# Kernel tuning notes

Hardware: AMD Instinct MI355X
Metric: run time of the kernel (lower is better)

Reference implementation:

```python
import jax, jax.numpy as jnp
import numpy as np

M, N, B, S = 512, 1024, 64, 50   # measurements, signal dim, batch, sparsity
TAU, ETA = 1.0, 0.1


def setup_inputs() -> dict:
    key = jax.random.key(0)
    k1, k2, k3 = jax.random.split(key, 3)
    X = jax.random.normal(k1, (N, B), dtype=jnp.float32)
    Y = jax.random.normal(k2, (B, M), dtype=jnp.float32)
    A = jax.random.normal(k3, (M, N), dtype=jnp.float32) / np.sqrt(M).astype(np.float32)
    W = jnp.ones((N,), dtype=jnp.float32)
    return {"X": X, "Y": Y, "A": A, "W": W}


def reference(X, Y, A, W):
    # Gradient step: H1 = (I - eta A^T A) X + eta A^T Y^T, computed without
    # materializing the N x N operator.  H1: (N, B)
    H1 = X - ETA * (A.T @ (A @ X)) + ETA * (A.T @ Y.T)
    # NeuralSort soft top-s mask per sample, batched over B.
    z = jnp.abs(W[:, None] * H1).T                      # (B, N) scores
    c = jnp.sum(jnp.abs(z[:, :, None] - z[:, None, :]), axis=-1)  # (B, N)
    ks = (N + 1 - 2 * jnp.arange(1, S + 1)).astype(z.dtype)       # (S,)
    logits = (ks[None, :, None] * z[:, None, :] - c[:, None, :]) / TAU  # (B, S, N)
    mask = jnp.sum(jax.nn.softmax(logits, axis=-1), axis=1)            # (B, N)
    return mask.T * H1                                  # (N, B)
```

## Files before the change

kernel.cpp:

```cpp
#include <hip/hip_runtime.h>
#include <math.h>

#define MM 512
#define NN 1024
#define BB 64
#define SS 50
#define ETA 0.1f

__global__ __launch_bounds__(512) void k_r(const float* __restrict__ X,
                                           const float* __restrict__ Y,
                                           const float* __restrict__ A,
                                           float* __restrict__ R_t) {
  const int l = threadIdx.x;
  const int w = threadIdx.y;
  const int m0 = blockIdx.x * 2;
  __shared__ float part[8][2][BB];
  const float* __restrict__ Xp = X + w * 128 * BB + l;
  const float* __restrict__ A0 = A + (size_t)m0 * NN + w * 128;
  const float* __restrict__ A1 = A0 + NN;
  float r0a = 0.f, r0b = 0.f, r1a = 0.f, r1b = 0.f;
  #pragma unroll 8
  for (int i = 0; i < 128; i += 4) {
    const float x0 = Xp[(i + 0) * BB];
    const float x1 = Xp[(i + 1) * BB];
    const float x2 = Xp[(i + 2) * BB];
    const float x3 = Xp[(i + 3) * BB];
    const float4 a0 = *reinterpret_cast<const float4*>(A0 + i);
    const float4 a1 = *reinterpret_cast<const float4*>(A1 + i);
    r0a = fmaf(a0.x, x0, fmaf(a0.y, x1, r0a));
    r0b = fmaf(a0.z, x2, fmaf(a0.w, x3, r0b));
    r1a = fmaf(a1.x, x0, fmaf(a1.y, x1, r1a));
    r1b = fmaf(a1.z, x2, fmaf(a1.w, x3, r1b));
  }
  part[w][0][l] = r0a + r0b;
  part[w][1][l] = r1a + r1b;
  __syncthreads();
  if (w == 0) {
    const float s0 =
        ((part[0][0][l] + part[1][0][l]) + (part[2][0][l] + part[3][0][l])) +
        ((part[4][0][l] + part[5][0][l]) + (part[6][0][l] + part[7][0][l]));
    const float s1 =
        ((part[0][1][l] + part[1][1][l]) + (part[2][1][l] + part[3][1][l])) +
        ((part[4][1][l] + part[5][1][l]) + (part[6][1][l] + part[7][1][l]));
    const float2 y2 = *reinterpret_cast<const float2*>(Y + l * MM + m0);
    *reinterpret_cast<float2*>(R_t + l * MM + m0) =
        make_float2(y2.x - s0, y2.y - s1);
  }
}

__global__ __launch_bounds__(512) void k_h1z(const float* __restrict__ X,
                                             const float* __restrict__ A,
                                             const float* __restrict__ R_t,
                                             const float* __restrict__ W,
                                             float* __restrict__ H1_t,
                                             float* __restrict__ z_t) {
  const int l = threadIdx.x;
  const int w = threadIdx.y;
  const int nc = blockIdx.x & 7;
  const int bp = blockIdx.x >> 3;
  const int t5 = w * 64 + l;
  __shared__ __align__(16) float Rs[2][MM];
  __shared__ float p2[2][4][128];

  if (t5 < 256) {
    const int row = t5 >> 7;
    const int idx = t5 & 127;
    reinterpret_cast<float4*>(Rs[row])[idx] =
        reinterpret_cast<const float4*>(R_t + (size_t)(bp * 2 + row) * MM)[idx];
  }
  __syncthreads();

  const int b_l = w >> 2;
  const int mc = w & 3;
  const int n0 = nc * 128;
  const float2* __restrict__ A2 =
      reinterpret_cast<const float2*>(A) + (size_t)(mc * 128) * (NN / 2) + n0 / 2 + l;
  const float4* __restrict__ R4 =
      reinterpret_cast<const float4*>(Rs[b_l]) + mc * 32;
  float s0 = 0.f, s1 = 0.f, s2 = 0.f, s3 = 0.f;
  float u0 = 0.f, u1 = 0.f, u2 = 0.f, u3 = 0.f;
  #pragma unroll 2
  for (int i = 0; i < 128; i += 4) {
    const float4 r = R4[i >> 2];
    const float2 q0 = A2[(size_t)(i + 0) * (NN / 2)];
    const float2 q1 = A2[(size_t)(i + 1) * (NN / 2)];
    const float2 q2 = A2[(size_t)(i + 2) * (NN / 2)];
    const float2 q3 = A2[(size_t)(i + 3) * (NN / 2)];
    s0 = fmaf(q0.x, r.x, s0); u0 = fmaf(q0.y, r.x, u0);
    s1 = fmaf(q1.x, r.y, s1); u1 = fmaf(q1.y, r.y, u1);
    s2 = fmaf(q2.x, r.z, s2); u2 = fmaf(q2.y, r.z, u2);
    s3 = fmaf(q3.x, r.w, s3); u3 = fmaf(q3.y, r.w, u3);
  }
  p2[b_l][mc][l * 2 + 0] = (s0 + s1) + (s2 + s3);
  p2[b_l][mc][l * 2 + 1] = (u0 + u1) + (u2 + u3);
  __syncthreads();
  if (t5 < 256) {
    const int bl2 = t5 >> 7;
    const int nn = t5 & 127;
    const int bb = bp * 2 + bl2;
    const int n = n0 + nn;
    const float s = (p2[bl2][0][nn] + p2[bl2][1][nn]) +
                    (p2[bl2][2][nn] + p2[bl2][3][nn]);
    const float h = fmaf(ETA, s, X[n * BB + bb]);
    H1_t[bb * NN + n] = h;
    z_t[bb * NN + n] = fabsf(W[n] * h);
  }
}

__global__ __launch_bounds__(256) void k_c(const float* __restrict__ z_t,
                                           float* __restrict__ c_part) {
  const int b = blockIdx.x >> 2;
  const int q = blockIdx.x & 3;
  const int t = threadIdx.x;
  __shared__ __align__(16) float4 z4[NN / 4];
  z4[t] = reinterpret_cast<const float4*>(z_t + b * NN)[t];
  __syncthreads();
  const float* zs = reinterpret_cast<const float*>(z4);
  const float zn0 = zs[t];
  const float zn1 = zs[t + 256];
  const float zn2 = zs[t + 512];
  const float zn3 = zs[t + 768];
  float c0 = 0.f, c1 = 0.f, c2 = 0.f, c3 = 0.f;
  const float4* zq = z4 + q * 64;
  #pragma unroll 4
  for (int i = 0; i < 64; ++i) {
    const float4 f = zq[i];
    c0 += (fabsf(zn0 - f.x) + fabsf(zn0 - f.y)) + (fabsf(zn0 - f.z) + fabsf(zn0 - f.w));
    c1 += (fabsf(zn1 - f.x) + fabsf(zn1 - f.y)) + (fabsf(zn1 - f.z) + fabsf(zn1 - f.w));
    c2 += (fabsf(zn2 - f.x) + fabsf(zn2 - f.y)) + (fabsf(zn2 - f.z) + fabsf(zn2 - f.w));
    c3 += (fabsf(zn3 - f.x) + fabsf(zn3 - f.y)) + (fabsf(zn3 - f.z) + fabsf(zn3 - f.w));
  }
  float* cp = c_part + (size_t)(b * 4 + q) * NN;
  cp[t] = c0;
  cp[t + 256] = c1;
  cp[t + 512] = c2;
  cp[t + 768] = c3;
}

__global__ __launch_bounds__(1024) void k_sm(const float* __restrict__ z_t,
                                             const float* __restrict__ c_part,
                                             const float* __restrict__ H1_t,
                                             float* __restrict__ out) {
  const int b = blockIdx.x;
  const int t = threadIdx.x;
  __shared__ __align__(16) float2 zc_s[NN];
  __shared__ float mpart[16][NN];

  const float* __restrict__ cb = c_part + (size_t)b * 4 * NN;
  const float c = (cb[t] + cb[t + NN]) + (cb[t + 2 * NN] + cb[t + 3 * NN]);
  zc_s[t] = make_float2(z_t[b * NN + t], c);
  const float h = H1_t[b * NN + t];
  __syncthreads();

  const int w = t >> 6;
  const int lane = t & 63;
  float zz[16], cc[16], mp[16];
  #pragma unroll
  for (int k = 0; k < 16; ++k) {
    const float2 v = zc_s[lane + 64 * k];
    zz[k] = v.x;
    cc[k] = v.y;
    mp[k] = 0.f;
  }

  for (int s = w; s < SS; s += 16) {
    const float ks = (float)(NN + 1 - 2 * (s + 1));
    float lg[16];
    float mx = -INFINITY;
    #pragma unroll
    for (int k = 0; k < 16; ++k) {
      lg[k] = fmaf(ks, zz[k], -cc[k]);
      mx = fmaxf(mx, lg[k]);
    }
    #pragma unroll
    for (int off = 32; off > 0; off >>= 1)
      mx = fmaxf(mx, __shfl_xor(mx, off, 64));
    float sum = 0.f;
    #pragma unroll
    for (int k = 0; k < 16; ++k) {
      lg[k] = __expf(lg[k] - mx);
      sum += lg[k];
    }
    #pragma unroll
    for (int off = 32; off > 0; off >>= 1)
      sum += __shfl_xor(sum, off, 64);
    const float rs = 1.f / sum;
    #pragma unroll
    for (int k = 0; k < 16; ++k) mp[k] = fmaf(lg[k], rs, mp[k]);
  }
  #pragma unroll
  for (int k = 0; k < 16; ++k) mpart[w][lane + 64 * k] = mp[k];
  __syncthreads();

  float mask = 0.f;
  #pragma unroll
  for (int u = 0; u < 16; ++u) mask += mpart[u][t];
  out[t * BB + b] = mask * h;
}

extern "C" void kernel_launch(void* const* d_in, const int* in_sizes, int n_in,
                              void* d_out, int out_size, void* d_ws, size_t ws_size,
                              hipStream_t stream) {
  const float* X = (const float*)d_in[0];
  const float* Y = (const float*)d_in[1];
  const float* A = (const float*)d_in[2];
  const float* W = (const float*)d_in[3];
  float* out = (float*)d_out;

  float* R_t = (float*)d_ws;
  float* z_t = R_t + BB * MM;
  float* H1_t = z_t + BB * NN;
  float* c_part = H1_t + BB * NN;

  k_r   <<<dim3(MM / 2), dim3(64, 8), 0, stream>>>(X, Y, A, R_t);
  k_h1z <<<dim3(256), dim3(64, 8), 0, stream>>>(X, A, R_t, W, H1_t, z_t);
  k_c   <<<dim3(BB * 4), dim3(256), 0, stream>>>(z_t, c_part);
  k_sm  <<<dim3(BB), dim3(1024), 0, stream>>>(z_t, c_part, H1_t, out);
}
```

Measured before the change: 35.69 us.

## Fuse H1, pairwise-distance and softmax stages into one dataflow kernel with counters

Merges the three kernels after the residual stage into a single launch. Block ranges play the producer or consumer role for each stage and hand off through device-scope atomic counters with spin-waits, which removes two launch gaps and lets later stages begin per batch column as soon as their inputs are ready. The k_r kernel zeroes the counters. The change depends on producer blocks being scheduled before or alongside the consumers that spin on them, and on all 576 blocks fitting co-resident on the device. Stores use atomic exchange and loads use atomic loads, which may cost more than plain memory ops. The softmax stage now uses 512 threads per block instead of 1024.

```diff
diff --git a/kernel.cpp b/kernel.cpp
--- a/kernel.cpp
+++ b/kernel.cpp
@@ -6,14 +6,38 @@
 #define BB 64
 #define SS 50
 #define ETA 0.1f
+#define AGENT __HIP_MEMORY_SCOPE_AGENT
+
+#define P_C0 256
+#define P_S0 512
+#define NPIPE 576
+
+__device__ __forceinline__ float aload(const float* p) {
+  return __hip_atomic_load(p, __ATOMIC_RELAXED, AGENT);
+}
+__device__ __forceinline__ void xstore(float* p, float v) {
+  (void)__hip_atomic_exchange(p, v, __ATOMIC_RELAXED, AGENT);
+}
+__device__ __forceinline__ void bump(unsigned* p) {
+  __hip_atomic_fetch_add(p, 1u, __ATOMIC_RELAXED, AGENT);
+}
+__device__ __forceinline__ void spin_ge(const unsigned* p, unsigned tgt) {
+  while (__hip_atomic_load(p, __ATOMIC_RELAXED, AGENT) < tgt)
+    __builtin_amdgcn_s_sleep(2);
+}
 
 __global__ __launch_bounds__(512) void k_r(const float* __restrict__ X,
                                            const float* __restrict__ Y,
                                            const float* __restrict__ A,
-                                           float* __restrict__ R_t) {
+                                           float* __restrict__ R_t,
+                                           unsigned* __restrict__ cnt) {
   const int l = threadIdx.x;
   const int w = threadIdx.y;
   const int m0 = blockIdx.x * 2;
+  if (blockIdx.x == 0) {
+    const int tid = w * 64 + l;
+    if (tid < 96) __hip_atomic_store(&cnt[tid], 0u, __ATOMIC_RELAXED, AGENT);
+  }
   __shared__ float part[8][2][BB];
   const float* __restrict__ Xp = X + w * 128 * BB + l;
   const float* __restrict__ A0 = A + (size_t)m0 * NN + w * 128;
@@ -48,154 +72,167 @@
   }
 }
 
-__global__ __launch_bounds__(512) void k_h1z(const float* __restrict__ X,
-                                             const float* __restrict__ A,
-                                             const float* __restrict__ R_t,
-                                             const float* __restrict__ W,
-                                             float* __restrict__ H1_t,
-                                             float* __restrict__ z_t) {
-  const int l = threadIdx.x;
-  const int w = threadIdx.y;
-  const int nc = blockIdx.x & 7;
-  const int bp = blockIdx.x >> 3;
-  const int t5 = w * 64 + l;
-  __shared__ __align__(16) float Rs[2][MM];
-  __shared__ float p2[2][4][128];
-
-  if (t5 < 256) {
-    const int row = t5 >> 7;
-    const int idx = t5 & 127;
-    reinterpret_cast<float4*>(Rs[row])[idx] =
-        reinterpret_cast<const float4*>(R_t + (size_t)(bp * 2 + row) * MM)[idx];
-  }
-  __syncthreads();
-
-  const int b_l = w >> 2;
-  const int mc = w & 3;
-  const int n0 = nc * 128;
-  const float2* __restrict__ A2 =
-      reinterpret_cast<const float2*>(A) + (size_t)(mc * 128) * (NN / 2) + n0 / 2 + l;
-  const float4* __restrict__ R4 =
-      reinterpret_cast<const float4*>(Rs[b_l]) + mc * 32;
-  float s0 = 0.f, s1 = 0.f, s2 = 0.f, s3 = 0.f;
-  float u0 = 0.f, u1 = 0.f, u2 = 0.f, u3 = 0.f;
-  #pragma unroll 2
-  for (int i = 0; i < 128; i += 4) {
-    const float4 r = R4[i >> 2];
-    const float2 q0 = A2[(size_t)(i + 0) * (NN / 2)];
-    const float2 q1 = A2[(size_t)(i + 1) * (NN / 2)];
-    const float2 q2 = A2[(size_t)(i + 2) * (NN / 2)];
-    const float2 q3 = A2[(size_t)(i + 3) * (NN / 2)];
-    s0 = fmaf(q0.x, r.x, s0); u0 = fmaf(q0.y, r.x, u0);
-    s1 = fmaf(q1.x, r.y, s1); u1 = fmaf(q1.y, r.y, u1);
-    s2 = fmaf(q2.x, r.z, s2); u2 = fmaf(q2.y, r.z, u2);
-    s3 = fmaf(q3.x, r.w, s3); u3 = fmaf(q3.y, r.w, u3);
-  }
-  p2[b_l][mc][l * 2 + 0] = (s0 + s1) + (s2 + s3);
-  p2[b_l][mc][l * 2 + 1] = (u0 + u1) + (u2 + u3);
-  __syncthreads();
-  if (t5 < 256) {
-    const int bl2 = t5 >> 7;
-    const int nn = t5 & 127;
-    const int bb = bp * 2 + bl2;
-    const int n = n0 + nn;
-    const float s = (p2[bl2][0][nn] + p2[bl2][1][nn]) +
-                    (p2[bl2][2][nn] + p2[bl2][3][nn]);
-    const float h = fmaf(ETA, s, X[n * BB + bb]);
-    H1_t[bb * NN + n] = h;
-    z_t[bb * NN + n] = fabsf(W[n] * h);
-  }
-}
-
-__global__ __launch_bounds__(256) void k_c(const float* __restrict__ z_t,
-                                           float* __restrict__ c_part) {
-  const int b = blockIdx.x >> 2;
-  const int q = blockIdx.x & 3;
+__global__ __launch_bounds__(512, 6) void k_pipe(
+    const float* __restrict__ X,
+    const float* __restrict__ A,
+    const float* __restrict__ R_t,
+    const float* __restrict__ W,
+    float* __restrict__ z_t,
+    float* __restrict__ H1_t,
+    float* __restrict__ c_part,
+    unsigned* __restrict__ cnt,
+    float* __restrict__ out) {
+  __shared__ __align__(16) char smem[40960];
+  const int bid = blockIdx.x;
   const int t = threadIdx.x;
-  __shared__ __align__(16) float4 z4[NN / 4];
-  z4[t] = reinterpret_cast<const float4*>(z_t + b * NN)[t];
-  __syncthreads();
-  const float* zs = reinterpret_cast<const float*>(z4);
-  const float zn0 = zs[t];
-  const float zn1 = zs[t + 256];
-  const float zn2 = zs[t + 512];
-  const float zn3 = zs[t + 768];
-  float c0 = 0.f, c1 = 0.f, c2 = 0.f, c3 = 0.f;
-  const float4* zq = z4 + q * 64;
-  #pragma unroll 4
-  for (int i = 0; i < 64; ++i) {
-    const float4 f = zq[i];
-    c0 += (fabsf(zn0 - f.x) + fabsf(zn0 - f.y)) + (fabsf(zn0 - f.z) + fabsf(zn0 - f.w));
-    c1 += (fabsf(zn1 - f.x) + fabsf(zn1 - f.y)) + (fabsf(zn1 - f.z) + fabsf(zn1 - f.w));
-    c2 += (fabsf(zn2 - f.x) + fabsf(zn2 - f.y)) + (fabsf(zn2 - f.z) + fabsf(zn2 - f.w));
-    c3 += (fabsf(zn3 - f.x) + fabsf(zn3 - f.y)) + (fabsf(zn3 - f.z) + fabsf(zn3 - f.w));
-  }
-  float* cp = c_part + (size_t)(b * 4 + q) * NN;
-  cp[t] = c0;
-  cp[t + 256] = c1;
-  cp[t + 512] = c2;
-  cp[t + 768] = c3;
-}
-
-__global__ __launch_bounds__(1024) void k_sm(const float* __restrict__ z_t,
-                                             const float* __restrict__ c_part,
-                                             const float* __restrict__ H1_t,
-                                             float* __restrict__ out) {
-  const int b = blockIdx.x;
-  const int t = threadIdx.x;
-  __shared__ __align__(16) float2 zc_s[NN];
-  __shared__ float mpart[16][NN];
-
-  const float* __restrict__ cb = c_part + (size_t)b * 4 * NN;
-  const float c = (cb[t] + cb[t + NN]) + (cb[t + 2 * NN] + cb[t + 3 * NN]);
-  zc_s[t] = make_float2(z_t[b * NN + t], c);
-  const float h = H1_t[b * NN + t];
-  __syncthreads();
-
+  const int l = t & 63;
   const int w = t >> 6;
-  const int lane = t & 63;
-  float zz[16], cc[16], mp[16];
-  #pragma unroll
-  for (int k = 0; k < 16; ++k) {
-    const float2 v = zc_s[lane + 64 * k];
-    zz[k] = v.x;
-    cc[k] = v.y;
-    mp[k] = 0.f;
-  }
-
-  for (int s = w; s < SS; s += 16) {
-    const float ks = (float)(NN + 1 - 2 * (s + 1));
-    float lg[16];
-    float mx = -INFINITY;
+  unsigned* cnt_h = cnt;
+  unsigned* cnt_c = cnt + 32;
+
+  if (bid < P_C0) {
+    const int nc = bid & 7;
+    const int bp = bid >> 3;
+    float* Rs = reinterpret_cast<float*>(smem);
+    float(*p2)[4][128] = reinterpret_cast<float(*)[4][128]>(smem + 4096);
+    Rs[t] = R_t[(size_t)(bp * 2) * MM + t];
+    Rs[512 + t] = R_t[(size_t)(bp * 2 + 1) * MM + t];
+    __syncthreads();
+    const int b_l = w >> 2;
+    const int mc = w & 3;
+    const int n0 = nc * 128;
+    const float2* __restrict__ A2 =
+        reinterpret_cast<const float2*>(A) + (size_t)(mc * 128) * (NN / 2) + n0 / 2 + l;
+    const float4* __restrict__ R4 =
+        reinterpret_cast<const float4*>(Rs + b_l * MM) + mc * 32;
+    float s0 = 0.f, s1 = 0.f, s2 = 0.f, s3 = 0.f;
+    float u0 = 0.f, u1 = 0.f, u2 = 0.f, u3 = 0.f;
+    #pragma unroll 2
+    for (int i = 0; i < 128; i += 4) {
+      const float4 r = R4[i >> 2];
+      const float2 q0 = A2[(size_t)(i + 0) * (NN / 2)];
+      const float2 q1 = A2[(size_t)(i + 1) * (NN / 2)];
+      const float2 q2 = A2[(size_t)(i + 2) * (NN / 2)];
+      const float2 q3 = A2[(size_t)(i + 3) * (NN / 2)];
+      s0 = fmaf(q0.x, r.x, s0); u0 = fmaf(q0.y, r.x, u0);
+      s1 = fmaf(q1.x, r.y, s1); u1 = fmaf(q1.y, r.y, u1);
+      s2 = fmaf(q2.x, r.z, s2); u2 = fmaf(q2.y, r.z, u2);
+      s3 = fmaf(q3.x, r.w, s3); u3 = fmaf(q3.y, r.w, u3);
+    }
+    p2[b_l][mc][l * 2 + 0] = (s0 + s1) + (s2 + s3);
+    p2[b_l][mc][l * 2 + 1] = (u0 + u1) + (u2 + u3);
+    __syncthreads();
+    if (t < 256) {
+      const int bl2 = t >> 7;
+      const int nn = t & 127;
+      const int bb = bp * 2 + bl2;
+      const int n = n0 + nn;
+      const float s = (p2[bl2][0][nn] + p2[bl2][1][nn]) +
+                      (p2[bl2][2][nn] + p2[bl2][3][nn]);
+      const float h = fmaf(ETA, s, X[n * BB + bb]);
+      xstore(&H1_t[bb * NN + n], h);
+      xstore(&z_t[bb * NN + n], fabsf(W[n] * h));
+    }
+    __syncthreads();
+    if (t == 0) bump(&cnt_h[bp]);
+
+  } else if (bid < P_S0) {
+    const int local = bid - P_C0;
+    const int b = local >> 2;
+    const int q = local & 3;
+    if (t == 0) spin_ge(&cnt_h[b >> 1], 8u);
+    __syncthreads();
+    float* zsf = reinterpret_cast<float*>(smem);
+    zsf[t] = aload(&z_t[b * NN + t]);
+    zsf[t + 512] = aload(&z_t[b * NN + t + 512]);
+    __syncthreads();
+    const float zn0 = zsf[t];
+    const float zn1 = zsf[t + 512];
+    float c0 = 0.f, c1 = 0.f;
+    const float4* zq = reinterpret_cast<const float4*>(zsf) + q * 64;
+    #pragma unroll 4
+    for (int i = 0; i < 64; ++i) {
+      const float4 f = zq[i];
+      c0 += (fabsf(zn0 - f.x) + fabsf(zn0 - f.y)) +
+            (fabsf(zn0 - f.z) + fabsf(zn0 - f.w));
+      c1 += (fabsf(zn1 - f.x) + fabsf(zn1 - f.y)) +
+            (fabsf(zn1 - f.z) + fabsf(zn1 - f.w));
+    }
+    float* cp = c_part + (size_t)(b * 4 + q) * NN;
+    xstore(cp + t, c0);
+    xstore(cp + t + 512, c1);
+    __syncthreads();
+    if (t == 0) bump(&cnt_c[b]);
+
+  } else {
+    const int b = bid - P_S0;
+    if (t == 0) {
+      spin_ge(&cnt_h[b >> 1], 8u);
+      spin_ge(&cnt_c[b], 4u);
+    }
+    __syncthreads();
+    float2* zc = reinterpret_cast<float2*>(smem);
+    float(*mpart)[NN] = reinterpret_cast<float(*)[NN]>(smem + 8192);
+    const float* __restrict__ cb = c_part + (size_t)b * 4 * NN;
+    {
+      const int i0 = t, i1 = t + 512;
+      const float cA = (aload(cb + i0) + aload(cb + i0 + NN)) +
+                       (aload(cb + i0 + 2 * NN) + aload(cb + i0 + 3 * NN));
+      const float cB = (aload(cb + i1) + aload(cb + i1 + NN)) +
+                       (aload(cb + i1 + 2 * NN) + aload(cb + i1 + 3 * NN));
+      zc[i0] = make_float2(aload(&z_t[b * NN + i0]), cA);
+      zc[i1] = make_float2(aload(&z_t[b * NN + i1]), cB);
+    }
+    const float h0 = aload(&H1_t[b * NN + t]);
+    const float h1 = aload(&H1_t[b * NN + t + 512]);
+    __syncthreads();
+
+    float zz[16], cc[16], mp[16];
     #pragma unroll
     for (int k = 0; k < 16; ++k) {
-      lg[k] = fmaf(ks, zz[k], -cc[k]);
-      mx = fmaxf(mx, lg[k]);
+      const float2 v = zc[l + 64 * k];
+      zz[k] = v.x;
+      cc[k] = v.y;
+      mp[k] = 0.f;
+    }
+    for (int s = w; s < SS; s += 8) {
+      const float ks = (float)(NN + 1 - 2 * (s + 1));
+      float lg[16];
+      float mx = -INFINITY;
+      #pragma unroll
+      for (int k = 0; k < 16; ++k) {
+        lg[k] = fmaf(ks, zz[k], -cc[k]);
+        mx = fmaxf(mx, lg[k]);
+      }
+      #pragma unroll
+      for (int off = 32; off > 0; off >>= 1)
+        mx = fmaxf(mx, __shfl_xor(mx, off, 64));
+      float sum = 0.f;
+      #pragma unroll
+      for (int k = 0; k < 16; ++k) {
+        lg[k] = __expf(lg[k] - mx);
+        sum += lg[k];
+      }
+      #pragma unroll
+      for (int off = 32; off > 0; off >>= 1)
+        sum += __shfl_xor(sum, off, 64);
+      const float rs = 1.f / sum;
+      #pragma unroll
+      for (int k = 0; k < 16; ++k) mp[k] = fmaf(lg[k], rs, mp[k]);
     }
     #pragma unroll
-    for (int off = 32; off > 0; off >>= 1)
-      mx = fmaxf(mx, __shfl_xor(mx, off, 64));
-    float sum = 0.f;
+    for (int k = 0; k < 16; ++k) mpart[w][l + 64 * k] = mp[k];
+    __syncthreads();
+
+    float m0 = 0.f, m1 = 0.f;
     #pragma unroll
-    for (int k = 0; k < 16; ++k) {
-      lg[k] = __expf(lg[k] - mx);
-      sum += lg[k];
-    }
-    #pragma unroll
-    for (int off = 32; off > 0; off >>= 1)
-      sum += __shfl_xor(sum, off, 64);
-    const float rs = 1.f / sum;
-    #pragma unroll
-    for (int k = 0; k < 16; ++k) mp[k] = fmaf(lg[k], rs, mp[k]);
-  }
-  #pragma unroll
-  for (int k = 0; k < 16; ++k) mpart[w][lane + 64 * k] = mp[k];
-  __syncthreads();
-
-  float mask = 0.f;
-  #pragma unroll
-  for (int u = 0; u < 16; ++u) mask += mpart[u][t];
-  out[t * BB + b] = mask * h;
+    for (int u = 0; u < 8; ++u) {
+      m0 += mpart[u][t];
+      m1 += mpart[u][t + 512];
+    }
+    out[t * BB + b] = m0 * h0;
+    out[(t + 512) * BB + b] = m1 * h1;
+  }
 }
 
 extern "C" void kernel_launch(void* const* d_in, const int* in_sizes, int n_in,
@@ -211,9 +248,9 @@
   float* z_t = R_t + BB * MM;
   float* H1_t = z_t + BB * NN;
   float* c_part = H1_t + BB * NN;
-
-  k_r   <<<dim3(MM / 2), dim3(64, 8), 0, stream>>>(X, Y, A, R_t);
-  k_h1z <<<dim3(256), dim3(64, 8), 0, stream>>>(X, A, R_t, W, H1_t, z_t);
-  k_c   <<<dim3(BB * 4), dim3(256), 0, stream>>>(z_t, c_part);
-  k_sm  <<<dim3(BB), dim3(1024), 0, stream>>>(z_t, c_part, H1_t, out);
-}
+  unsigned* cnt = (unsigned*)(c_part + 4 * BB * NN);
+
+  k_r   <<<dim3(MM / 2), dim3(64, 8), 0, stream>>>(X, Y, A, R_t, cnt);
+  k_pipe<<<dim3(NPIPE), dim3(512), 0, stream>>>(X, A, R_t, W, z_t, H1_t,
+                                                c_part, cnt, out);
+}
```

Result: slower. 51.04 us (+43.0%).

## Compute pairwise abs-diff sums via bitonic sort and prefix sums inside softmax kernel

Applied to the files above, without the earlier changes.

Replaces the O(N^2) pairwise |z_i - z_j| reduction kernel with an in-block bitonic sort of z followed by a prefix-sum closed form for c. That computation is fused into the softmax kernel, which removes one launch and the c_part round trip through global memory. It also raises the unroll factor of the A^T R loop. The sort needs many __syncthreads across 1024 threads, and the closed form can round differently from the direct sum, with ties broken by index.

```diff
diff --git a/kernel.cpp b/kernel.cpp
--- a/kernel.cpp
+++ b/kernel.cpp
@@ -79,7 +79,7 @@
       reinterpret_cast<const float4*>(Rs[b_l]) + mc * 32;
   float s0 = 0.f, s1 = 0.f, s2 = 0.f, s3 = 0.f;
   float u0 = 0.f, u1 = 0.f, u2 = 0.f, u3 = 0.f;
-  #pragma unroll 2
+  #pragma unroll 4
   for (int i = 0; i < 128; i += 4) {
     const float4 r = R4[i >> 2];
     const float2 q0 = A2[(size_t)(i + 0) * (NN / 2)];
@@ -107,62 +107,76 @@
   }
 }
 
-__global__ __launch_bounds__(256) void k_c(const float* __restrict__ z_t,
-                                           float* __restrict__ c_part) {
-  const int b = blockIdx.x >> 2;
-  const int q = blockIdx.x & 3;
-  const int t = threadIdx.x;
-  __shared__ __align__(16) float4 z4[NN / 4];
-  z4[t] = reinterpret_cast<const float4*>(z_t + b * NN)[t];
-  __syncthreads();
-  const float* zs = reinterpret_cast<const float*>(z4);
-  const float zn0 = zs[t];
-  const float zn1 = zs[t + 256];
-  const float zn2 = zs[t + 512];
-  const float zn3 = zs[t + 768];
-  float c0 = 0.f, c1 = 0.f, c2 = 0.f, c3 = 0.f;
-  const float4* zq = z4 + q * 64;
-  #pragma unroll 4
-  for (int i = 0; i < 64; ++i) {
-    const float4 f = zq[i];
-    c0 += (fabsf(zn0 - f.x) + fabsf(zn0 - f.y)) + (fabsf(zn0 - f.z) + fabsf(zn0 - f.w));
-    c1 += (fabsf(zn1 - f.x) + fabsf(zn1 - f.y)) + (fabsf(zn1 - f.z) + fabsf(zn1 - f.w));
-    c2 += (fabsf(zn2 - f.x) + fabsf(zn2 - f.y)) + (fabsf(zn2 - f.z) + fabsf(zn2 - f.w));
-    c3 += (fabsf(zn3 - f.x) + fabsf(zn3 - f.y)) + (fabsf(zn3 - f.z) + fabsf(zn3 - f.w));
-  }
-  float* cp = c_part + (size_t)(b * 4 + q) * NN;
-  cp[t] = c0;
-  cp[t + 256] = c1;
-  cp[t + 512] = c2;
-  cp[t + 768] = c3;
-}
-
-__global__ __launch_bounds__(1024) void k_sm(const float* __restrict__ z_t,
-                                             const float* __restrict__ c_part,
-                                             const float* __restrict__ H1_t,
-                                             float* __restrict__ out) {
+__global__ __launch_bounds__(1024) void k_smc(const float* __restrict__ z_t,
+                                              const float* __restrict__ H1_t,
+                                              float* __restrict__ out) {
   const int b = blockIdx.x;
   const int t = threadIdx.x;
-  __shared__ __align__(16) float2 zc_s[NN];
+  const int l = t & 63;
+  const int w = t >> 6;
+  __shared__ float zs[NN];
+  __shared__ float sv[NN];
+  __shared__ int si[NN];
+  __shared__ float wsum[16];
   __shared__ float mpart[16][NN];
 
-  const float* __restrict__ cb = c_part + (size_t)b * 4 * NN;
-  const float c = (cb[t] + cb[t + NN]) + (cb[t + 2 * NN] + cb[t + 3 * NN]);
-  zc_s[t] = make_float2(z_t[b * NN + t], c);
+  const float zval = z_t[b * NN + t];
   const float h = H1_t[b * NN + t];
-  __syncthreads();
-
-  const int w = t >> 6;
-  const int lane = t & 63;
+  zs[t] = zval;
+
+  float v = zval;
+  int idx = t;
+  for (int k = 2; k <= NN; k <<= 1) {
+    for (int j = k >> 1; j > 0; j >>= 1) {
+      float pv;
+      int pi;
+      if (j >= 64) {
+        __syncthreads();
+        sv[t] = v;
+        si[t] = idx;
+        __syncthreads();
+        pv = sv[t ^ j];
+        pi = si[t ^ j];
+      } else {
+        pv = __shfl_xor(v, j, 64);
+        pi = __shfl_xor(idx, j, 64);
+      }
+      const bool want_min = (((t & j) == 0) == ((t & k) == 0));
+      const bool mine_less = (v < pv) || (v == pv && idx < pi);
+      if (want_min != mine_less) {
+        v = pv;
+        idx = pi;
+      }
+    }
+  }
+
+  float p = v;
+  #pragma unroll
+  for (int d = 1; d < 64; d <<= 1) {
+    const float pu = __shfl_up(p, d, 64);
+    if (l >= d) p += pu;
+  }
+  if (l == 63) wsum[w] = p;
+  __syncthreads();
+  float off = 0.f, S = 0.f;
+  #pragma unroll
+  for (int u = 0; u < 16; ++u) {
+    const float ws = wsum[u];
+    if (u < w) off += ws;
+    S += ws;
+  }
+  const float P = p + off;
+  const float c = fmaf((float)(2 * t + 2 - NN), v, S - 2.f * P);
+  sv[idx] = c;
+  __syncthreads();
+
   float zz[16], cc[16], mp[16];
   #pragma unroll
   for (int k = 0; k < 16; ++k) {
-    const float2 v = zc_s[lane + 64 * k];
-    zz[k] = v.x;
-    cc[k] = v.y;
+    zz[k] = zs[l + 64 * k];
+    cc[k] = sv[l + 64 * k];
     mp[k] = 0.f;
   }
-
   for (int s = w; s < SS; s += 16) {
     const float ks = (float)(NN + 1 - 2 * (s + 1));
     float lg[16];
@@ -173,8 +187,8 @@
       mx = fmaxf(mx, lg[k]);
     }
     #pragma unroll
-    for (int off = 32; off > 0; off >>= 1)
-      mx = fmaxf(mx, __shfl_xor(mx, off, 64));
+    for (int off2 = 32; off2 > 0; off2 >>= 1)
+      mx = fmaxf(mx, __shfl_xor(mx, off2, 64));
     float sum = 0.f;
     #pragma unroll
     for (int k = 0; k < 16; ++k) {
@@ -182,14 +196,14 @@
       sum += lg[k];
     }
     #pragma unroll
-    for (int off = 32; off > 0; off >>= 1)
-      sum += __shfl_xor(sum, off, 64);
+    for (int off2 = 32; off2 > 0; off2 >>= 1)
+      sum += __shfl_xor(sum, off2, 64);
     const float rs = 1.f / sum;
     #pragma unroll
     for (int k = 0; k < 16; ++k) mp[k] = fmaf(lg[k], rs, mp[k]);
   }
   #pragma unroll
-  for (int k = 0; k < 16; ++k) mpart[w][lane + 64 * k] = mp[k];
+  for (int k = 0; k < 16; ++k) mpart[w][l + 64 * k] = mp[k];
   __syncthreads();
 
   float mask = 0.f;
@@ -210,10 +224,8 @@
   float* R_t = (float*)d_ws;
   float* z_t = R_t + BB * MM;
   float* H1_t = z_t + BB * NN;
-  float* c_part = H1_t + BB * NN;
 
   k_r   <<<dim3(MM / 2), dim3(64, 8), 0, stream>>>(X, Y, A, R_t);
   k_h1z <<<dim3(256), dim3(64, 8), 0, stream>>>(X, A, R_t, W, H1_t, z_t);
-  k_c   <<<dim3(BB * 4), dim3(256), 0, stream>>>(z_t, c_part);
-  k_sm  <<<dim3(BB), dim3(1024), 0, stream>>>(z_t, c_part, H1_t, out);
-}
+  k_smc <<<dim3(BB), dim3(1024), 0, stream>>>(z_t, H1_t, out);
+}
```

Result: slower. 38.37 us (+7.5%).
